# Performance work log

Hardware: AMD Instinct MI355X
Metric: run time of the kernel (lower is better)

The kernel has to match this reference:

```python
import jax, jax.numpy as jnp
import numpy as np

N_ROBOTS = 32   # len(cfg.ENV.WALKERS)
SEQ = 12        # cfg.MODEL.MAX_LIMBS
LOBS = 52       # per-limb proprioceptive obs size
HID = 256       # cfg.MODEL.MLP.HIDDEN_DIM
LOUT = 2        # out_dim // SEQ
BATCH = 1024


def _uniform(k, shape, r):
    return jax.random.uniform(k, shape, jnp.float32, -r, r)


def setup_inputs() -> dict:
    key = jax.random.key(0)
    ks = jax.random.split(key, 14)
    obs = jax.random.normal(ks[0], (BATCH, SEQ * LOBS), jnp.float32)
    obs_mask = jax.random.randint(ks[1], (BATCH, SEQ), 0, 2).astype(bool)
    unimal_ids = jax.random.randint(ks[2], (BATCH,), 0, N_ROBOTS).astype(jnp.int32)
    ir_in, ir = 0.04, 1.0 / 16
    return {
        "obs": obs,
        "obs_mask": obs_mask,
        "unimal_ids": unimal_ids,
        "Wi": _uniform(ks[3], (N_ROBOTS, SEQ, LOBS, HID), ir_in),
        "bi": _uniform(ks[4], (N_ROBOTS, SEQ, HID), ir_in / SEQ),
        "W1": _uniform(ks[5], (N_ROBOTS, HID, HID), ir),
        "b1": _uniform(ks[6], (N_ROBOTS, HID), ir),
        "W2": _uniform(ks[7], (N_ROBOTS, HID, HID), ir),
        "b2": _uniform(ks[8], (N_ROBOTS, HID), ir),
        "W3": _uniform(ks[9], (N_ROBOTS, HID, HID), ir),
        "b3": _uniform(ks[10], (N_ROBOTS, HID), ir),
        "Wo": _uniform(ks[11], (N_ROBOTS, SEQ, HID, LOUT), ir),
        "bo": _uniform(ks[12], (N_ROBOTS, SEQ, LOUT), ir),
    }


def reference(obs, obs_mask, unimal_ids, Wi, bi, W1, b1, W2, b2, W3, b3, Wo, bo):
    B = obs.shape[0]
    o3 = obs.reshape(B, SEQ, LOBS)
    # HN_INPUT branch: per-robot input hypernetwork weights
    emb = jnp.einsum("bsl,bslh->bsh", o3, Wi[unimal_ids]) + bi[unimal_ids]
    emb = emb * (1.0 - obs_mask.astype(emb.dtype))[:, :, None]
    emb = jax.nn.relu(emb.sum(axis=1))  # [B, HID]
    # PER_ROBOT_HIDDEN_LAYERS: three per-robot dense layers
    emb = jax.nn.relu(jnp.einsum("bh,bhk->bk", emb, W1[unimal_ids]) + b1[unimal_ids])
    emb = jax.nn.relu(jnp.einsum("bh,bhk->bk", emb, W2[unimal_ids]) + b2[unimal_ids])
    emb = jax.nn.relu(jnp.einsum("bh,bhk->bk", emb, W3[unimal_ids]) + b3[unimal_ids])
    # HN_OUTPUT branch: per-robot, per-limb output hypernetwork
    out = jnp.einsum("bh,bshd->bsd", emb, Wo[unimal_ids]) + bo[unimal_ids]
    return out.reshape(B, -1)  # [B, SEQ*LOUT]
```

## Files before the change

### kernel.cpp

```cpp
#include <hip/hip_runtime.h>

#define NROB 32
#define SEQ 12
#define LOBS 52
#define HID 256
#define LOUT 2
#define BATCH 1024
#define KIN 624
#define SPB 8
#define NSD 24
#define NBLK 320
#define SLOTS 40

__device__ __forceinline__ void fma4(float4& a, const float4 w, const float s) {
  a.x = fmaf(w.x, s, a.x);
  a.y = fmaf(w.y, s, a.y);
  a.z = fmaf(w.z, s, a.z);
  a.w = fmaf(w.w, s, a.w);
}

template <int ROWS, int SX>
__device__ __forceinline__ void stream4(const float* __restrict__ wp,
                                        const float* xb, float4* acc) {
  static_assert(ROWS % 8 == 0, "ROWS multiple of 8");
  constexpr int G = ROWS / 8;
  float4 w[8];
#pragma unroll
  for (int j = 0; j < 8; ++j) w[j] = *(const float4*)(wp + j * HID);
  wp += 8 * HID;
#pragma unroll
  for (int g = 0; g < G; ++g) {
    float4 nw[8];
    if (g + 1 < G) {
#pragma unroll
      for (int j = 0; j < 8; ++j) nw[j] = *(const float4*)(wp + j * HID);
      wp += 8 * HID;
    }
#pragma unroll
    for (int i = 0; i < 4; ++i) {
      const float4 xa = *(const float4*)(xb + i * SX + g * 8);
      const float4 xc = *(const float4*)(xb + i * SX + g * 8 + 4);
      fma4(acc[i], w[0], xa.x);
      fma4(acc[i], w[1], xa.y);
      fma4(acc[i], w[2], xa.z);
      fma4(acc[i], w[3], xa.w);
      fma4(acc[i], w[4], xc.x);
      fma4(acc[i], w[5], xc.y);
      fma4(acc[i], w[6], xc.z);
      fma4(acc[i], w[7], xc.w);
    }
#pragma unroll
    for (int j = 0; j < 8; ++j) w[j] = nw[j];
  }
}

__global__ __launch_bounds__(1024, 4) void k_fused(
    const float* __restrict__ obs, const int* __restrict__ mask,
    const int* __restrict__ ids, const float* __restrict__ Wi,
    const float* __restrict__ bi, const float* __restrict__ W1,
    const float* __restrict__ b1, const float* __restrict__ W2,
    const float* __restrict__ b2, const float* __restrict__ W3,
    const float* __restrict__ b3, const float* __restrict__ Wo,
    const float* __restrict__ bo, float* __restrict__ out) {
  __shared__ int s_cnt[NROB];
  __shared__ int s_wc[16];
  __shared__ int s_bm[SPB], s_vm[SPB], s_mb[SPB];
  __shared__ float s_ind[SPB][SEQ];
  __shared__ __align__(16) float s_x0[SPB * KIN];
  __shared__ __align__(16) float s_P[4][SPB][HID];
  __shared__ __align__(16) float s_x1[SPB][HID];

  const int t = threadIdx.x;
  const int bx = blockIdx.x;

  if (t < NROB) s_cnt[t] = 0;
  if (t < SPB) s_bm[t] = 0;
  __syncthreads();
  const int id0 = ids[t];
  atomicAdd(&s_cnt[id0], 1);
  __syncthreads();

  int myr = -1, mybase = 0;
  {
    int maxbucket = 0;
    for (int x = 0; x < 8; ++x) {
      int bsum = 0;
      for (int r = x; r < NROB; r += 8) bsum += (s_cnt[r] + SPB - 1) >> 3;
      maxbucket = max(maxbucket, bsum);
    }
    if (maxbucket <= SLOTS) {
      const int myxcd = bx & 7, myslot = bx >> 3;
      int slot = 0;
      for (int r = myxcd; r < NROB; r += 8) {
        const int nch = (s_cnt[r] + SPB - 1) >> 3;
        if (myr < 0 && myslot >= slot && myslot < slot + nch) {
          myr = r;
          mybase = (myslot - slot) * SPB;
        }
        slot += nch;
      }
    } else {
      int ch = 0;
      for (int r = 0; r < NROB; ++r) {
        const int nch = (s_cnt[r] + SPB - 1) >> 3;
        if (myr < 0 && bx >= ch && bx < ch + nch) {
          myr = r;
          mybase = (bx - ch) * SPB;
        }
        ch += nch;
      }
    }
  }
  if (myr < 0) return;
  const int mycnt = s_cnt[myr];

  {
    const int wv = t >> 6;
    const unsigned lane = t & 63;
    const unsigned long long m0 = __ballot(id0 == myr);
    if (lane == 0) s_wc[wv] = __popcll(m0);
    __syncthreads();
    int pre = 0;
    for (int i = 0; i < wv; ++i) pre += s_wc[i];
    if (id0 == myr) {
      const unsigned long long below = (1ull << lane) - 1ull;
      const int j = pre + __popcll(m0 & below) - mybase;
      if (j >= 0 && j < SPB) s_bm[j] = t;
    }
    __syncthreads();
  }
  if (t < SPB) {
    const int v = (mybase + t) < mycnt;
    s_vm[t] = v;
    int mb = 0xFFF;
    if (v) {
      mb = 0;
      const int b = s_bm[t];
      for (int s = 0; s < SEQ; ++s) mb |= (mask[b * SEQ + s] != 0) << s;
    }
    s_mb[t] = mb;
  }
  if (t >= 64 && t < 64 + SPB * SEQ) {
  }
  __syncthreads();
  if (t < SPB * SEQ) {
    const int m = t / SEQ, s = t - m * SEQ;
    s_ind[m][s] = ((s_mb[m] >> s) & 1) ? 0.f : 1.f;
  }
  for (int q = t; q < SPB * (KIN / 4); q += 1024) {
    const int m = q / 156, f4 = q - m * 156;
    const int s = f4 / 13;
    float4 v = {0.f, 0.f, 0.f, 0.f};
    if (!((s_mb[m] >> s) & 1))
      v = *(const float4*)(obs + (size_t)s_bm[m] * KIN + f4 * 4);
    *(float4*)&s_x0[m * KIN + f4 * 4] = v;
  }
  __syncthreads();

  const int w = t >> 6, lane = t & 63;
  const int seg = w >> 1, sg = w & 1;
  float* Pp = &s_P[seg & 3][sg * 4][lane * 4];

  {
    float4 acc[4];
#pragma unroll
    for (int i = 0; i < 4; ++i) acc[i] = {0.f, 0.f, 0.f, 0.f};
    const float* Wr = Wi + ((size_t)myr * KIN + seg * 80) * HID + lane * 4;
    const float* xb = &s_x0[(sg * 4) * KIN + seg * 80];
    if (seg < 7)
      stream4<80, KIN>(Wr, xb, acc);
    else
      stream4<64, KIN>(Wr, xb, acc);
    if (seg < 4) {
#pragma unroll
      for (int i = 0; i < 4; ++i) *(float4*)(Pp + i * HID) = acc[i];
    }
    __syncthreads();
    if (seg >= 4) {
#pragma unroll
      for (int i = 0; i < 4; ++i) {
        float4 c = *(const float4*)(Pp + i * HID);
        c.x += acc[i].x;
        c.y += acc[i].y;
        c.z += acc[i].z;
        c.w += acc[i].w;
        *(float4*)(Pp + i * HID) = c;
      }
    }
    __syncthreads();
    {
      const int m = t >> 7, c2 = (t & 127) * 2;
      float2 a = {0.f, 0.f};
#pragma unroll
      for (int j = 0; j < 4; ++j) {
        const float2 p = *(const float2*)&s_P[j][m][c2];
        a.x += p.x;
        a.y += p.y;
      }
      const float* br = bi + (size_t)myr * SEQ * HID + c2;
#pragma unroll
      for (int s = 0; s < SEQ; ++s) {
        const float2 b2v = *(const float2*)(br + s * HID);
        const float f = s_ind[m][s];
        a.x = fmaf(b2v.x, f, a.x);
        a.y = fmaf(b2v.y, f, a.y);
      }
      s_x1[m][c2] = fmaxf(a.x, 0.f);
      s_x1[m][c2 + 1] = fmaxf(a.y, 0.f);
    }
    __syncthreads();
  }

  float* X2 = s_x0;
  const float* Ws[3] = {W1, W2, W3};
  const float* bs[3] = {b1, b2, b3};
#pragma unroll
  for (int L = 0; L < 3; ++L) {
    const float* Xin = (L & 1) ? X2 : &s_x1[0][0];
    float* Xout = (L & 1) ? &s_x1[0][0] : X2;
    float4 acc[4];
#pragma unroll
    for (int i = 0; i < 4; ++i) acc[i] = {0.f, 0.f, 0.f, 0.f};
    const float* Wr = Ws[L] + ((size_t)myr * HID + seg * 32) * HID + lane * 4;
    stream4<32, HID>(Wr, Xin + (sg * 4) * HID + seg * 32, acc);
    if (seg < 4) {
#pragma unroll
      for (int i = 0; i < 4; ++i) *(float4*)(Pp + i * HID) = acc[i];
    }
    __syncthreads();
    if (seg >= 4) {
#pragma unroll
      for (int i = 0; i < 4; ++i) {
        float4 c = *(const float4*)(Pp + i * HID);
        c.x += acc[i].x;
        c.y += acc[i].y;
        c.z += acc[i].z;
        c.w += acc[i].w;
        *(float4*)(Pp + i * HID) = c;
      }
    }
    __syncthreads();
    {
      const int m = t >> 7, c2 = (t & 127) * 2;
      float2 a = {0.f, 0.f};
#pragma unroll
      for (int j = 0; j < 4; ++j) {
        const float2 p = *(const float2*)&s_P[j][m][c2];
        a.x += p.x;
        a.y += p.y;
      }
      const float2 bv = *(const float2*)(bs[L] + (size_t)myr * HID + c2);
      Xout[m * HID + c2] = fmaxf(a.x + bv.x, 0.f);
      Xout[m * HID + c2 + 1] = fmaxf(a.y + bv.y, 0.f);
    }
    __syncthreads();
  }

  float* S = &s_P[0][0][0];
  {
    const float* Wop = Wo + (size_t)myr * SEQ * HID * LOUT;
    for (int q = t; q < (NSD * HID) / 4; q += 1024) {
      const float4 v = *(const float4*)(Wop + q * 4);
      const int flat = q * 4;
      const int s = flat >> 9;
      const int k = (flat & 511) >> 1;
      S[(k + 0) * 25 + s * 2 + 0] = v.x;
      S[(k + 0) * 25 + s * 2 + 1] = v.y;
      S[(k + 1) * 25 + s * 2 + 0] = v.z;
      S[(k + 1) * 25 + s * 2 + 1] = v.w;
    }
  }
  __syncthreads();
  if (t < SPB * NSD) {
    const int m = t / NSD, sd = t - m * NSD;
    float a = bo[(size_t)myr * NSD + sd];
    const float* xp = X2 + m * HID;
#pragma unroll 8
    for (int k = 0; k < HID; ++k) a = fmaf(xp[k], S[k * 25 + sd], a);
    if (s_vm[m]) out[(size_t)s_bm[m] * NSD + sd] = a;
  }
}

extern "C" void kernel_launch(void* const* d_in, const int* in_sizes, int n_in,
                              void* d_out, int out_size, void* d_ws, size_t ws_size,
                              hipStream_t stream) {
  const float* obs = (const float*)d_in[0];
  const int* mask = (const int*)d_in[1];
  const int* ids = (const int*)d_in[2];
  const float* Wi = (const float*)d_in[3];
  const float* bi = (const float*)d_in[4];
  const float* W1 = (const float*)d_in[5];
  const float* b1 = (const float*)d_in[6];
  const float* W2 = (const float*)d_in[7];
  const float* b2 = (const float*)d_in[8];
  const float* W3 = (const float*)d_in[9];
  const float* b3 = (const float*)d_in[10];
  const float* Wo = (const float*)d_in[11];
  const float* bo = (const float*)d_in[12];
  float* out = (float*)d_out;
  (void)d_ws;
  hipLaunchKernelGGL(k_fused, dim3(NBLK), dim3(1024), 0, stream, obs, mask, ids,
                     Wi, bi, W1, b1, W2, b2, W3, b3, Wo, bo, out);
}
```

Measured before the change: 40.35 us.

## Have each wave handle all 8 samples and halve the grid to 160 blocks

Each wave now multiplies its weight rows against all 8 samples in the block, where before it covered 4. Every weight element loaded from global memory is therefore reused twice as often, and the K range is split across 16 waves instead of 8 segment pairs. Slots per block drop from 40 to 20 and the grid from 320 to 160 blocks, which reduces redundant weight streaming across blocks. In exchange it needs more accumulator registers, a 4-round serialized shared-memory reduction with extra barriers, and a single shared arena that aliases the buffers; fewer blocks may also leave some CUs idle.

```diff
diff --git a/kernel.cpp b/kernel.cpp
--- a/kernel.cpp
+++ b/kernel.cpp
@@ -9,8 +9,12 @@
 #define KIN 624
 #define SPB 8
 #define NSD 24
-#define NBLK 320
-#define SLOTS 40
+#define NBLK 160
+#define SLOTS 20
+
+#define OFF_P 4992
+#define OFF_X1 13184
+#define ARENA_F 15232
 
 __device__ __forceinline__ void fma4(float4& a, const float4 w, const float s) {
   a.x = fmaf(w.x, s, a.x);
@@ -19,38 +23,45 @@
   a.w = fmaf(w.w, s, a.w);
 }
 
-template <int ROWS, int SX>
-__device__ __forceinline__ void stream4(const float* __restrict__ wp,
+template <int ROWS, int XS>
+__device__ __forceinline__ void stream8(const float* __restrict__ wp,
                                         const float* xb, float4* acc) {
   static_assert(ROWS % 8 == 0, "ROWS multiple of 8");
-  constexpr int G = ROWS / 8;
-  float4 w[8];
-#pragma unroll
-  for (int j = 0; j < 8; ++j) w[j] = *(const float4*)(wp + j * HID);
-  wp += 8 * HID;
-#pragma unroll
-  for (int g = 0; g < G; ++g) {
-    float4 nw[8];
-    if (g + 1 < G) {
-#pragma unroll
-      for (int j = 0; j < 8; ++j) nw[j] = *(const float4*)(wp + j * HID);
-      wp += 8 * HID;
-    }
-#pragma unroll
-    for (int i = 0; i < 4; ++i) {
-      const float4 xa = *(const float4*)(xb + i * SX + g * 8);
-      const float4 xc = *(const float4*)(xb + i * SX + g * 8 + 4);
-      fma4(acc[i], w[0], xa.x);
-      fma4(acc[i], w[1], xa.y);
-      fma4(acc[i], w[2], xa.z);
-      fma4(acc[i], w[3], xa.w);
-      fma4(acc[i], w[4], xc.x);
-      fma4(acc[i], w[5], xc.y);
-      fma4(acc[i], w[6], xc.z);
-      fma4(acc[i], w[7], xc.w);
-    }
-#pragma unroll
-    for (int j = 0; j < 8; ++j) w[j] = nw[j];
+  constexpr int G = ROWS / 4;
+  float4 A[4], B[4];
+#pragma unroll
+  for (int j = 0; j < 4; ++j) A[j] = *(const float4*)(wp + j * HID);
+#pragma unroll
+  for (int j = 0; j < 4; ++j) B[j] = *(const float4*)(wp + (4 + j) * HID);
+#pragma unroll
+  for (int g = 0; g < G; g += 2) {
+    const int k = g * 4;
+#pragma unroll
+    for (int m = 0; m < SPB; ++m) {
+      const float4 x = *(const float4*)(xb + m * XS + k);
+      fma4(acc[m], A[0], x.x);
+      fma4(acc[m], A[1], x.y);
+      fma4(acc[m], A[2], x.z);
+      fma4(acc[m], A[3], x.w);
+    }
+    if (g + 2 < G) {
+#pragma unroll
+      for (int j = 0; j < 4; ++j)
+        A[j] = *(const float4*)(wp + (size_t)(k + 8 + j) * HID);
+    }
+#pragma unroll
+    for (int m = 0; m < SPB; ++m) {
+      const float4 x = *(const float4*)(xb + m * XS + k + 4);
+      fma4(acc[m], B[0], x.x);
+      fma4(acc[m], B[1], x.y);
+      fma4(acc[m], B[2], x.z);
+      fma4(acc[m], B[3], x.w);
+    }
+    if (g + 3 < G) {
+#pragma unroll
+      for (int j = 0; j < 4; ++j)
+        B[j] = *(const float4*)(wp + (size_t)(k + 12 + j) * HID);
+    }
   }
 }
 
@@ -66,9 +77,11 @@
   __shared__ int s_wc[16];
   __shared__ int s_bm[SPB], s_vm[SPB], s_mb[SPB];
   __shared__ float s_ind[SPB][SEQ];
-  __shared__ __align__(16) float s_x0[SPB * KIN];
-  __shared__ __align__(16) float s_P[4][SPB][HID];
-  __shared__ __align__(16) float s_x1[SPB][HID];
+  __shared__ __align__(16) float sm[ARENA_F];
+  float* x0 = sm;
+  float* P = sm + OFF_P;
+  float* x1 = sm + OFF_X1;
+  float* x2 = sm;
 
   const int t = threadIdx.x;
   const int bx = blockIdx.x;
@@ -140,8 +153,6 @@
     }
     s_mb[t] = mb;
   }
-  if (t >= 64 && t < 64 + SPB * SEQ) {
-  }
   __syncthreads();
   if (t < SPB * SEQ) {
     const int m = t / SEQ, s = t - m * SEQ;
@@ -153,47 +164,49 @@
     float4 v = {0.f, 0.f, 0.f, 0.f};
     if (!((s_mb[m] >> s) & 1))
       v = *(const float4*)(obs + (size_t)s_bm[m] * KIN + f4 * 4);
-    *(float4*)&s_x0[m * KIN + f4 * 4] = v;
+    *(float4*)&x0[m * KIN + f4 * 4] = v;
   }
   __syncthreads();
 
   const int w = t >> 6, lane = t & 63;
-  const int seg = w >> 1, sg = w & 1;
-  float* Pp = &s_P[seg & 3][sg * 4][lane * 4];
+  float* Pw = P + (w & 3) * (SPB * HID) + lane * 4;
 
   {
-    float4 acc[4];
-#pragma unroll
-    for (int i = 0; i < 4; ++i) acc[i] = {0.f, 0.f, 0.f, 0.f};
-    const float* Wr = Wi + ((size_t)myr * KIN + seg * 80) * HID + lane * 4;
-    const float* xb = &s_x0[(sg * 4) * KIN + seg * 80];
-    if (seg < 7)
-      stream4<80, KIN>(Wr, xb, acc);
+    float4 acc[SPB];
+#pragma unroll
+    for (int m = 0; m < SPB; ++m) acc[m] = {0.f, 0.f, 0.f, 0.f};
+    const float* Wr = Wi + ((size_t)myr * KIN + w * 40) * HID + lane * 4;
+    const float* xb = x0 + w * 40;
+    if (w < 15)
+      stream8<40, KIN>(Wr, xb, acc);
     else
-      stream4<64, KIN>(Wr, xb, acc);
-    if (seg < 4) {
-#pragma unroll
-      for (int i = 0; i < 4; ++i) *(float4*)(Pp + i * HID) = acc[i];
-    }
-    __syncthreads();
-    if (seg >= 4) {
-#pragma unroll
-      for (int i = 0; i < 4; ++i) {
-        float4 c = *(const float4*)(Pp + i * HID);
-        c.x += acc[i].x;
-        c.y += acc[i].y;
-        c.z += acc[i].z;
-        c.w += acc[i].w;
-        *(float4*)(Pp + i * HID) = c;
-      }
-    }
-    __syncthreads();
+      stream8<24, KIN>(Wr, xb, acc);
+    if (w < 4) {
+#pragma unroll
+      for (int m = 0; m < SPB; ++m) *(float4*)(Pw + m * HID) = acc[m];
+    }
+    __syncthreads();
+#pragma unroll
+    for (int rnd = 1; rnd < 4; ++rnd) {
+      if ((w >> 2) == rnd) {
+#pragma unroll
+        for (int m = 0; m < SPB; ++m) {
+          float4 c = *(const float4*)(Pw + m * HID);
+          c.x += acc[m].x;
+          c.y += acc[m].y;
+          c.z += acc[m].z;
+          c.w += acc[m].w;
+          *(float4*)(Pw + m * HID) = c;
+        }
+      }
+      __syncthreads();
+    }
     {
       const int m = t >> 7, c2 = (t & 127) * 2;
       float2 a = {0.f, 0.f};
 #pragma unroll
       for (int j = 0; j < 4; ++j) {
-        const float2 p = *(const float2*)&s_P[j][m][c2];
+        const float2 p = *(const float2*)&P[(j * SPB + m) * HID + c2];
         a.x += p.x;
         a.y += p.y;
       }
@@ -205,47 +218,49 @@
         a.x = fmaf(b2v.x, f, a.x);
         a.y = fmaf(b2v.y, f, a.y);
       }
-      s_x1[m][c2] = fmaxf(a.x, 0.f);
-      s_x1[m][c2 + 1] = fmaxf(a.y, 0.f);
-    }
-    __syncthreads();
-  }
-
-  float* X2 = s_x0;
+      x1[m * HID + c2] = fmaxf(a.x, 0.f);
+      x1[m * HID + c2 + 1] = fmaxf(a.y, 0.f);
+    }
+    __syncthreads();
+  }
+
   const float* Ws[3] = {W1, W2, W3};
   const float* bs[3] = {b1, b2, b3};
 #pragma unroll
   for (int L = 0; L < 3; ++L) {
-    const float* Xin = (L & 1) ? X2 : &s_x1[0][0];
-    float* Xout = (L & 1) ? &s_x1[0][0] : X2;
-    float4 acc[4];
-#pragma unroll
-    for (int i = 0; i < 4; ++i) acc[i] = {0.f, 0.f, 0.f, 0.f};
-    const float* Wr = Ws[L] + ((size_t)myr * HID + seg * 32) * HID + lane * 4;
-    stream4<32, HID>(Wr, Xin + (sg * 4) * HID + seg * 32, acc);
-    if (seg < 4) {
-#pragma unroll
-      for (int i = 0; i < 4; ++i) *(float4*)(Pp + i * HID) = acc[i];
-    }
-    __syncthreads();
-    if (seg >= 4) {
-#pragma unroll
-      for (int i = 0; i < 4; ++i) {
-        float4 c = *(const float4*)(Pp + i * HID);
-        c.x += acc[i].x;
-        c.y += acc[i].y;
-        c.z += acc[i].z;
-        c.w += acc[i].w;
-        *(float4*)(Pp + i * HID) = c;
-      }
-    }
-    __syncthreads();
+    const float* Xin = (L & 1) ? x2 : x1;
+    float* Xout = (L & 1) ? x1 : x2;
+    float4 acc[SPB];
+#pragma unroll
+    for (int m = 0; m < SPB; ++m) acc[m] = {0.f, 0.f, 0.f, 0.f};
+    const float* Wr = Ws[L] + ((size_t)myr * HID + w * 16) * HID + lane * 4;
+    stream8<16, HID>(Wr, Xin + w * 16, acc);
+    if (w < 4) {
+#pragma unroll
+      for (int m = 0; m < SPB; ++m) *(float4*)(Pw + m * HID) = acc[m];
+    }
+    __syncthreads();
+#pragma unroll
+    for (int rnd = 1; rnd < 4; ++rnd) {
+      if ((w >> 2) == rnd) {
+#pragma unroll
+        for (int m = 0; m < SPB; ++m) {
+          float4 c = *(const float4*)(Pw + m * HID);
+          c.x += acc[m].x;
+          c.y += acc[m].y;
+          c.z += acc[m].z;
+          c.w += acc[m].w;
+          *(float4*)(Pw + m * HID) = c;
+        }
+      }
+      __syncthreads();
+    }
     {
       const int m = t >> 7, c2 = (t & 127) * 2;
       float2 a = {0.f, 0.f};
 #pragma unroll
       for (int j = 0; j < 4; ++j) {
-        const float2 p = *(const float2*)&s_P[j][m][c2];
+        const float2 p = *(const float2*)&P[(j * SPB + m) * HID + c2];
         a.x += p.x;
         a.y += p.y;
       }
@@ -256,7 +271,7 @@
     __syncthreads();
   }
 
-  float* S = &s_P[0][0][0];
+  float* S = P;
   {
     const float* Wop = Wo + (size_t)myr * SEQ * HID * LOUT;
     for (int q = t; q < (NSD * HID) / 4; q += 1024) {
@@ -274,7 +289,7 @@
   if (t < SPB * NSD) {
     const int m = t / NSD, sd = t - m * NSD;
     float a = bo[(size_t)myr * NSD + sd];
-    const float* xp = X2 + m * HID;
+    const float* xp = x2 + m * HID;
 #pragma unroll 8
     for (int k = 0; k < HID; ++k) a = fmaf(xp[k], S[k * 25 + sd], a);
     if (s_vm[m]) out[(size_t)s_bm[m] * NSD + sd] = a;
@@ -299,6 +314,7 @@
   const float* bo = (const float*)d_in[12];
   float* out = (float*)d_out;
   (void)d_ws;
-  hipLaunchKernelGGL(k_fused, dim3(NBLK), dim3(1024), 0, stream, obs, mask, ids,
-                     Wi, bi, W1, b1, W2, b2, W3, b3, Wo, bo, out);
+
+  hipLaunchKernelGGL(k_fused, dim3(NBLK), dim3(1024), 0, stream, obs, mask,
+                     ids, Wi, bi, W1, b1, W2, b2, W3, b3, Wo, bo, out);
 }
```

After: 51.62 us. 27.9% more time.
